# Kernel optimization log

Hardware: AMD Instinct MI355X
Metric: run time of the kernel (lower is better)

Reference implementation:

```python
import jax, jax.numpy as jnp
import numpy as np

B, S, W = 128, 256, 1
DEPTH = 655            # MathTypeKeysMax
UNITS = 128
PROBLEM_BUCKETS = 32


def setup_inputs() -> dict:
    key = jax.random.key(0)
    ks = jax.random.split(key, 14)
    ri = lambda k, shape, hi: jax.random.randint(k, shape, 0, hi, dtype=jnp.int32)
    K = 4 * DEPTH * W  # flattened per-timestep feature width = 2620
    return {
        'move_count': ri(ks[0], (B,), 100),
        'moves_remaining': ri(ks[1], (B,), 100),
        'last_rule': ri(ks[2], (B,), 12),
        'node_count': ri(ks[3], (B,), 64),
        'problem_type': ri(ks[4], (B,), PROBLEM_BUCKETS),
        'bwd_vectors': ri(ks[5], (B, S, W), DEPTH),
        'fwd_vectors': ri(ks[6], (B, S, W), DEPTH),
        'last_bwd_vectors': ri(ks[7], (B, S, W), DEPTH),
        'last_fwd_vectors': ri(ks[8], (B, S, W), DEPTH),
        'W_dense': jax.random.normal(ks[9], (K, UNITS), jnp.float32) * (1.0 / np.sqrt(K)),
        'b_dense': jnp.zeros((UNITS,), jnp.float32),
        'Wx': jax.random.normal(ks[10], (UNITS, 4 * UNITS), jnp.float32) * (1.0 / np.sqrt(UNITS)),
        'Wh': jax.random.normal(ks[11], (UNITS, 4 * UNITS), jnp.float32) * (1.0 / np.sqrt(UNITS)),
        'b_lstm': jnp.zeros((4 * UNITS,), jnp.float32),
    }


def _lstm(x, Wx, Wh, b):
    # x: [B, S, U] -> (seq hidden [B, S, U], final hidden [B, U]); keras gate order i,f,c,o
    U = Wh.shape[0]
    bsz = x.shape[0]
    # precompute input projections once: [S, B, 4U]
    xz = jnp.einsum('bsu,uv->sbv', x, Wx) + b

    def step(carry, zt):
        h, c = carry
        z = zt + h @ Wh
        i, f, g, o = jnp.split(z, 4, axis=-1)
        i = jax.nn.sigmoid(i)
        f = jax.nn.sigmoid(f)
        g = jnp.tanh(g)
        o = jax.nn.sigmoid(o)
        c = f * c + i * g
        h = o * jnp.tanh(c)
        return (h, c), h

    init = (jnp.zeros((bsz, U), x.dtype), jnp.zeros((bsz, U), x.dtype))
    (h_last, _), hs = jax.lax.scan(step, init, xz)
    return jnp.transpose(hs, (1, 0, 2)), h_last


def reference(move_count, moves_remaining, last_rule, node_count, problem_type,
              bwd_vectors, fwd_vectors, last_bwd_vectors, last_fwd_vectors,
              W_dense, b_dense, Wx, Wh, b_lstm):
    f32 = lambda a: a.astype(jnp.float32)
    # DenseFeatures context extraction: 3 numeric int columns + 32-bucket indicator
    context_inputs = jnp.concatenate([
        f32(last_rule)[:, None],
        f32(move_count)[:, None],
        f32(node_count)[:, None],
        jax.nn.one_hot(problem_type, PROBLEM_BUCKETS, dtype=jnp.float32),
    ], axis=-1)  # [B, 35]

    sequence_length = bwd_vectors.shape[1]
    # one-hot each [B,S,W] sequence to [B,S,W,DEPTH], concat on last axis -> [B,S,W,4*DEPTH]
    oh = jnp.concatenate([
        jax.nn.one_hot(bwd_vectors, DEPTH, dtype=jnp.float32),
        jax.nn.one_hot(fwd_vectors, DEPTH, dtype=jnp.float32),
        jax.nn.one_hot(last_bwd_vectors, DEPTH, dtype=jnp.float32),
        jax.nn.one_hot(last_fwd_vectors, DEPTH, dtype=jnp.float32),
    ], axis=-1)
    bsz = oh.shape[0]
    # per-example Flatten keeps leading S dim, so the loop == one batched matmul
    flat = oh.reshape(bsz, sequence_length, -1)      # [B, S, 4*DEPTH*W]
    outputs = jnp.einsum('bsk,ku->bsu', flat, W_dense) + b_dense  # [B, S, U]

    hidden_states, lstm_vectors = _lstm(outputs, Wx, Wh, b_lstm)
    return (context_inputs, lstm_vectors, hidden_states, sequence_length)
```

## Files before the change

kernel.cpp:

```cpp
#include <hip/hip_runtime.h>
#include <cstdint>

#define BB   128
#define SS   256
#define NDEPTH 655
#define UU   128
#define VV   512
#define NPB  32

__global__ void context_kernel(const int* __restrict__ last_rule,
                               const int* __restrict__ move_count,
                               const int* __restrict__ node_count,
                               const int* __restrict__ problem_type,
                               float* __restrict__ out, int write_seq) {
    int i = blockIdx.x * blockDim.x + threadIdx.x;
    if (i < BB * 35) {
        int b = i / 35, c = i % 35;
        float v;
        if (c == 0)      v = (float)last_rule[b];
        else if (c == 1) v = (float)move_count[b];
        else if (c == 2) v = (float)node_count[b];
        else             v = (problem_type[b] == (c - 3)) ? 1.0f : 0.0f;
        out[i] = v;
    }
    if (write_seq && i == 0)
        out[(size_t)BB*35 + (size_t)BB*UU + (size_t)BB*SS*UU] = (float)SS;
}

__global__ void wdwx_kernel(const float* __restrict__ Wd,
                            const float* __restrict__ Wx,
                            const float* __restrict__ b_dense,
                            const float* __restrict__ b_lstm,
                            float* __restrict__ WdWx,
                            float* __restrict__ base) {
    int v  = threadIdx.x;
    int k0 = blockIdx.x * 4;
    const float* wd0 = Wd + (size_t)k0 * UU;
    float a0 = 0.f, a1 = 0.f, a2 = 0.f, a3 = 0.f;
    for (int u = 0; u < UU; ++u) {
        float wx = Wx[u * VV + v];
        a0 = fmaf(wd0[u],        wx, a0);
        a1 = fmaf(wd0[UU + u],   wx, a1);
        a2 = fmaf(wd0[2*UU + u], wx, a2);
        a3 = fmaf(wd0[3*UU + u], wx, a3);
    }
    WdWx[(size_t)(k0+0)*VV + v] = a0;
    WdWx[(size_t)(k0+1)*VV + v] = a1;
    WdWx[(size_t)(k0+2)*VV + v] = a2;
    WdWx[(size_t)(k0+3)*VV + v] = a3;
    if (blockIdx.x == 0) {
        float a = 0.f;
        for (int u = 0; u < UU; ++u) a = fmaf(b_dense[u], Wx[u * VV + v], a);
        base[v] = a + b_lstm[v];
    }
}

__global__ __launch_bounds__(512, 2)
void lstm_kernel(const int* __restrict__ bwd,  const int* __restrict__ fwd,
                 const int* __restrict__ lbwd, const int* __restrict__ lfwd,
                 const float* __restrict__ WdWx,
                 const float* __restrict__ base,
                 const float* __restrict__ Wh,
                 float* __restrict__ hidden_states,
                 float* __restrict__ lstm_vectors) {
    const int b    = blockIdx.x;
    const int t    = threadIdx.x;
    const int lane = t & 63;
    const int w    = t >> 6;
    const int q    = lane & 3;
    const int u    = w * 16 + (lane >> 2);
    const int col  = q * UU + u;

    __shared__ __align__(16) float h_buf[2][144];
    __shared__ int idx_lds[SS][4];

    float wh[128];
    #pragma unroll
    for (int kk = 0; kk < 32; ++kk) {
        #pragma unroll
        for (int g = 0; g < 4; ++g)
            wh[kk*4+g] = Wh[(size_t)(32*q + kk) * VV + g*UU + u];
    }

    for (int s = t; s < SS; s += 512) {
        idx_lds[s][0] =            bwd [b*SS + s];
        idx_lds[s][1] =   NDEPTH + fwd [b*SS + s];
        idx_lds[s][2] = 2*NDEPTH + lbwd[b*SS + s];
        idx_lds[s][3] = 3*NDEPTH + lfwd[b*SS + s];
    }
    if (t < UU) h_buf[0][36*(t>>5) + (t&31)] = 0.0f;
    float c    = 0.0f;
    float bias = base[col];
    __syncthreads();

    float g0 = WdWx[(size_t)idx_lds[0][0] * VV + col];
    float g1 = WdWx[(size_t)idx_lds[0][1] * VV + col];
    float g2 = WdWx[(size_t)idx_lds[0][2] * VV + col];
    float g3 = WdWx[(size_t)idx_lds[0][3] * VV + col];

    const bool b0 = (q & 1) != 0;
    const bool b1 = (q & 2) != 0;

    int p = 0;
    for (int s = 0; s < SS; ++s) {
        float z = bias + (g0 + g1) + (g2 + g3);
        if (s + 1 < SS) {
            g0 = WdWx[(size_t)idx_lds[s+1][0] * VV + col];
            g1 = WdWx[(size_t)idx_lds[s+1][1] * VV + col];
            g2 = WdWx[(size_t)idx_lds[s+1][2] * VV + col];
            g3 = WdWx[(size_t)idx_lds[s+1][3] * VV + col];
        }

        const float* hb = h_buf[p] + 36 * q;
        float pp0 = 0.f, pp1 = 0.f, pp2 = 0.f, pp3 = 0.f;
        #pragma unroll
        for (int kk = 0; kk < 32; kk += 4) {
            float4 hv = *(const float4*)(hb + kk);
            pp0 = fmaf(hv.x, wh[(kk+0)*4+0], pp0);
            pp1 = fmaf(hv.x, wh[(kk+0)*4+1], pp1);
            pp2 = fmaf(hv.x, wh[(kk+0)*4+2], pp2);
            pp3 = fmaf(hv.x, wh[(kk+0)*4+3], pp3);
            pp0 = fmaf(hv.y, wh[(kk+1)*4+0], pp0);
            pp1 = fmaf(hv.y, wh[(kk+1)*4+1], pp1);
            pp2 = fmaf(hv.y, wh[(kk+1)*4+2], pp2);
            pp3 = fmaf(hv.y, wh[(kk+1)*4+3], pp3);
            pp0 = fmaf(hv.z, wh[(kk+2)*4+0], pp0);
            pp1 = fmaf(hv.z, wh[(kk+2)*4+1], pp1);
            pp2 = fmaf(hv.z, wh[(kk+2)*4+2], pp2);
            pp3 = fmaf(hv.z, wh[(kk+2)*4+3], pp3);
            pp0 = fmaf(hv.w, wh[(kk+3)*4+0], pp0);
            pp1 = fmaf(hv.w, wh[(kk+3)*4+1], pp1);
            pp2 = fmaf(hv.w, wh[(kk+3)*4+2], pp2);
            pp3 = fmaf(hv.w, wh[(kk+3)*4+3], pp3);
        }

        float keepA = b0 ? pp1 : pp0;
        float keepB = b0 ? pp3 : pp2;
        float sendA = b0 ? pp0 : pp1;
        float sendB = b0 ? pp2 : pp3;
        float sA = keepA + __shfl_xor(sendA, 1);
        float sB = keepB + __shfl_xor(sendB, 1);
        float send2 = b1 ? sA : sB;
        z += (b1 ? sB : sA) + __shfl_xor(send2, 2);

        float xs = (q == 2) ? 2.0f * z : z;
        float sg = __fdividef(1.0f, 1.0f + __expf(-xs));
        float a  = (q == 2) ? 2.0f * sg - 1.0f : sg;

        float v1 = __shfl_xor(a, 1);
        float v2 = __shfl_xor(a, 2);
        float v3 = __shfl_xor(v1, 2);
        float ig = (q & 1) ? v1 * v3 : a * v2;
        float gf = (q & 1) ? ((q & 2) ? v2 : a)
                           : ((q & 2) ? v3 : v1);
        float go = (q & 1) ? ((q & 2) ? a  : v2)
                           : ((q & 2) ? v1 : v3);
        c = fmaf(gf, c, ig);
        float e  = __expf(2.0f * c);
        float tc = 1.0f - __fdividef(2.0f, e + 1.0f);
        float h  = go * tc;

        if (q == 0) {
            h_buf[p ^ 1][36*(u>>5) + (u&31)] = h;
            hidden_states[((size_t)b * SS + s) * UU + u] = h;
        }
        __syncthreads();
        p ^= 1;
    }
    if (t < UU) lstm_vectors[(size_t)b * UU + t] = h_buf[p][36*(t>>5) + (t&31)];
}

extern "C" void kernel_launch(void* const* d_in, const int* in_sizes, int n_in,
                              void* d_out, int out_size, void* d_ws, size_t ws_size,
                              hipStream_t stream) {
    const int* move_count   = (const int*)d_in[0];
    const int* last_rule    = (const int*)d_in[2];
    const int* node_count   = (const int*)d_in[3];
    const int* problem_type = (const int*)d_in[4];
    const int* bwd          = (const int*)d_in[5];
    const int* fwd          = (const int*)d_in[6];
    const int* lbwd         = (const int*)d_in[7];
    const int* lfwd         = (const int*)d_in[8];
    const float* Wd         = (const float*)d_in[9];
    const float* b_dense    = (const float*)d_in[10];
    const float* Wx         = (const float*)d_in[11];
    const float* Wh         = (const float*)d_in[12];
    const float* b_lstm     = (const float*)d_in[13];

    float* out  = (float*)d_out;
    float* WdWx = (float*)d_ws;
    float* base = WdWx + (size_t)(4 * NDEPTH) * VV;

    float* lstm_out = out + BB * 35;
    float* hs_out   = lstm_out + BB * UU;
    int write_seq = (out_size > BB*35 + BB*UU + BB*SS*UU) ? 1 : 0;

    context_kernel<<<(BB*35 + 255)/256, 256, 0, stream>>>(
        last_rule, move_count, node_count, problem_type, out, write_seq);
    wdwx_kernel<<<NDEPTH, VV, 0, stream>>>(Wd, Wx, b_dense, b_lstm, WdWx, base);
    lstm_kernel<<<BB, 512, 0, stream>>>(bwd, fwd, lbwd, lfwd, WdWx, base, Wh,
                                        hs_out, lstm_out);
}
```

Measured before the change: 312.6 us.

## Split LSTM recurrent dot product across 8 lanes with 1024-thread blocks

Doubles the threads per batch-row block from 512 to 1024 so each hidden unit's recurrent matmul is split across 8 lanes (16 K-elements each) instead of 4 (32 each). Each thread now holds half as many Wh registers and gathers two of the four WdWx rows per step instead of four, with an extra xor-4 shuffle combining the two halves. This shortens the serial per-step critical path of the 256-step recurrence at the cost of more threads per barrier, an extra shuffle, and redundant activation math.

```diff
diff --git a/kernel.cpp b/kernel.cpp
--- a/kernel.cpp
+++ b/kernel.cpp
@@ -55,7 +55,7 @@
     }
 }
 
-__global__ __launch_bounds__(512, 2)
+__global__ __launch_bounds__(1024, 4)
 void lstm_kernel(const int* __restrict__ bwd,  const int* __restrict__ fwd,
                  const int* __restrict__ lbwd, const int* __restrict__ lfwd,
                  const float* __restrict__ WdWx,
@@ -68,53 +68,54 @@
     const int lane = t & 63;
     const int w    = t >> 6;
     const int q    = lane & 3;
-    const int u    = w * 16 + (lane >> 2);
+    const int e    = (lane >> 2) & 1;
+    const int u    = w * 8 + (lane >> 3);
     const int col  = q * UU + u;
-
-    __shared__ __align__(16) float h_buf[2][144];
+    const int ch   = q + 4 * e;
+
+    __shared__ __align__(16) float h_buf[2][160];
     __shared__ int idx_lds[SS][4];
 
-    float wh[128];
+    float wh[64];
     #pragma unroll
-    for (int kk = 0; kk < 32; ++kk) {
+    for (int kk = 0; kk < 16; ++kk) {
         #pragma unroll
         for (int g = 0; g < 4; ++g)
-            wh[kk*4+g] = Wh[(size_t)(32*q + kk) * VV + g*UU + u];
-    }
-
-    for (int s = t; s < SS; s += 512) {
+            wh[kk*4+g] = Wh[(size_t)(16*ch + kk) * VV + g*UU + u];
+    }
+
+    for (int s = t; s < SS; s += 1024) {
         idx_lds[s][0] =            bwd [b*SS + s];
         idx_lds[s][1] =   NDEPTH + fwd [b*SS + s];
         idx_lds[s][2] = 2*NDEPTH + lbwd[b*SS + s];
         idx_lds[s][3] = 3*NDEPTH + lfwd[b*SS + s];
     }
-    if (t < UU) h_buf[0][36*(t>>5) + (t&31)] = 0.0f;
+    if (t < UU) h_buf[0][20*(t>>4) + (t&15)] = 0.0f;
     float c    = 0.0f;
     float bias = base[col];
     __syncthreads();
 
-    float g0 = WdWx[(size_t)idx_lds[0][0] * VV + col];
-    float g1 = WdWx[(size_t)idx_lds[0][1] * VV + col];
-    float g2 = WdWx[(size_t)idx_lds[0][2] * VV + col];
-    float g3 = WdWx[(size_t)idx_lds[0][3] * VV + col];
+    float g0 = WdWx[(size_t)idx_lds[0][2*e    ] * VV + col];
+    float g1 = WdWx[(size_t)idx_lds[0][2*e + 1] * VV + col];
 
     const bool b0 = (q & 1) != 0;
     const bool b1 = (q & 2) != 0;
 
     int p = 0;
     for (int s = 0; s < SS; ++s) {
-        float z = bias + (g0 + g1) + (g2 + g3);
+        float gsum = g0 + g1;
         if (s + 1 < SS) {
-            g0 = WdWx[(size_t)idx_lds[s+1][0] * VV + col];
-            g1 = WdWx[(size_t)idx_lds[s+1][1] * VV + col];
-            g2 = WdWx[(size_t)idx_lds[s+1][2] * VV + col];
-            g3 = WdWx[(size_t)idx_lds[s+1][3] * VV + col];
+            g0 = WdWx[(size_t)idx_lds[s+1][2*e    ] * VV + col];
+            g1 = WdWx[(size_t)idx_lds[s+1][2*e + 1] * VV + col];
         }
 
-        const float* hb = h_buf[p] + 36 * q;
-        float pp0 = 0.f, pp1 = 0.f, pp2 = 0.f, pp3 = 0.f;
+        float pp0 = (q == 0) ? gsum : 0.f;
+        float pp1 = (q == 1) ? gsum : 0.f;
+        float pp2 = (q == 2) ? gsum : 0.f;
+        float pp3 = (q == 3) ? gsum : 0.f;
+        const float* hb = h_buf[p] + 20 * ch;
         #pragma unroll
-        for (int kk = 0; kk < 32; kk += 4) {
+        for (int kk = 0; kk < 16; kk += 4) {
             float4 hv = *(const float4*)(hb + kk);
             pp0 = fmaf(hv.x, wh[(kk+0)*4+0], pp0);
             pp1 = fmaf(hv.x, wh[(kk+0)*4+1], pp1);
@@ -141,7 +142,8 @@
         float sA = keepA + __shfl_xor(sendA, 1);
         float sB = keepB + __shfl_xor(sendB, 1);
         float send2 = b1 ? sA : sB;
-        z += (b1 ? sB : sA) + __shfl_xor(send2, 2);
+        float zh = (b1 ? sB : sA) + __shfl_xor(send2, 2);
+        float z = bias + zh + __shfl_xor(zh, 4);
 
         float xs = (q == 2) ? 2.0f * z : z;
         float sg = __fdividef(1.0f, 1.0f + __expf(-xs));
@@ -156,18 +158,18 @@
         float go = (q & 1) ? ((q & 2) ? a  : v2)
                            : ((q & 2) ? v1 : v3);
         c = fmaf(gf, c, ig);
-        float e  = __expf(2.0f * c);
-        float tc = 1.0f - __fdividef(2.0f, e + 1.0f);
+        float ex = __expf(2.0f * c);
+        float tc = 1.0f - __fdividef(2.0f, ex + 1.0f);
         float h  = go * tc;
 
-        if (q == 0) {
-            h_buf[p ^ 1][36*(u>>5) + (u&31)] = h;
+        if ((lane & 7) == 0) {
+            h_buf[p ^ 1][20*(u>>4) + (u&15)] = h;
             hidden_states[((size_t)b * SS + s) * UU + u] = h;
         }
         __syncthreads();
         p ^= 1;
     }
-    if (t < UU) lstm_vectors[(size_t)b * UU + t] = h_buf[p][36*(t>>5) + (t&31)];
+    if (t < UU) lstm_vectors[(size_t)b * UU + t] = h_buf[p][20*(t>>4) + (t&15)];
 }
 
 extern "C" void kernel_launch(void* const* d_in, const int* in_sizes, int n_in,
@@ -198,6 +200,6 @@
     context_kernel<<<(BB*35 + 255)/256, 256, 0, stream>>>(
         last_rule, move_count, node_count, problem_type, out, write_seq);
     wdwx_kernel<<<NDEPTH, VV, 0, stream>>>(Wd, Wx, b_dense, b_lstm, WdWx, base);
-    lstm_kernel<<<BB, 512, 0, stream>>>(bwd, fwd, lbwd, lfwd, WdWx, base, Wh,
-                                        hs_out, lstm_out);
-}
+    lstm_kernel<<<BB, 1024, 0, stream>>>(bwd, fwd, lbwd, lfwd, WdWx, base, Wh,
+                                         hs_out, lstm_out);
+}
```

New measurement: 343.2 us. 9.8% more time.
